# Kernel optimization log

Measured on AMD Instinct MI355X. Metric: run time of the kernel, lower is better.

The kernel has to match this reference:

```python
import jax, jax.numpy as jnp
import numpy as np

D = 1024      # d_model
H = 16        # nhead
DH = D // H   # d_head = 64
DC = D // 4   # d_compress = 256
HID = 2048    # dim_feedforward (SwiGLU hidden)
G = 2         # num_groups
EPG = 4       # experts_per_gp
E = G * EPG   # num_experts = 8
TOPK = 2
EPS = 1e-6
B, T = 2, 2048


def _rope_sincos(t, dh):
    inv_freq = 1.0 / (10000.0 ** (jnp.arange(0, dh, 2, dtype=jnp.float32) / dh))
    ang = jnp.arange(t, dtype=jnp.float32)[:, None] * inv_freq[None, :]  # [T, dh/2]
    return jnp.sin(ang), jnp.cos(ang)


def _apply_rope(x, sin, cos):
    # x: [B, H, T, DH]; sin/cos: [T, DH/2] broadcast over B,H
    x1 = x[..., ::2]
    x2 = x[..., 1::2]
    r = jnp.stack([x1 * cos - x2 * sin, x1 * sin + x2 * cos], axis=-1)
    return r.reshape(x.shape)


def _swiglu(x):
    a, b = jnp.split(x, 2, axis=-1)
    return jax.nn.silu(a) * b


def _rmsnorm(x, w):
    return x * jax.lax.rsqrt(jnp.mean(x * x, axis=-1, keepdims=True) + EPS) * w


def reference(src, Wq, Wk_c, Wv_c, Wk, Wv, Wo,
              W_shared_in, W_shared_out, W1_shared, W2_experts,
              Wg_gate, We_gate, group_bias, expert_bias, norm1_w, norm2_w):
    Bb, Tt, C = src.shape
    # ---- Latent attention (K/V compressed to d_c then re-expanded) ----
    q = (src @ Wq).reshape(Bb, Tt, H, DH).transpose(0, 2, 1, 3)
    k = ((src @ Wk_c) @ Wk).reshape(Bb, Tt, H, DH).transpose(0, 2, 1, 3)
    v = ((src @ Wv_c) @ Wv).reshape(Bb, Tt, H, DH).transpose(0, 2, 1, 3)
    sin, cos = _rope_sincos(Tt, DH)
    q = _apply_rope(q, sin, cos)
    k = _apply_rope(k, sin, cos)
    attn = jnp.einsum('bhqd,bhkd->bhqk', q, k) / np.sqrt(DH).astype(np.float32)
    attn = jax.nn.softmax(attn, axis=-1)
    sa = jnp.einsum('bhqk,bhkd->bhqd', attn, v)
    sa = sa.transpose(0, 2, 1, 3).reshape(Bb, Tt, C) @ Wo
    x = _rmsnorm(src + sa, norm1_w)

    # ---- Hierarchical MoE FFN ----
    S = Bb * Tt
    flat = x.reshape(S, C)
    shared = _swiglu(flat @ W_shared_in) @ W_shared_out          # [S, C]
    g_probs = jax.nn.softmax(flat @ Wg_gate + group_bias, -1)    # [S, G]
    g_idx = jnp.argmax(g_probs, axis=-1)                          # [S]
    e_logits = flat @ We_gate + expert_bias                       # [S, E]
    e_group = jnp.arange(E) // EPG
    in_group = e_group[None, :] == g_idx[:, None]                 # [S, E]
    e_probs = jax.nn.softmax(jnp.where(in_group, e_logits, -jnp.inf), -1)
    g_prob = jnp.take_along_axis(g_probs, g_idx[:, None], axis=1)  # [S, 1]
    p_expert = e_probs * g_prob
    topv, topi = jax.lax.top_k(p_expert, TOPK)                    # [S, K]
    # dense combine weights: zero for non-selected experts (same math as dispatch loop)
    w = jnp.zeros((S, E), flat.dtype).at[jnp.arange(S)[:, None], topi].set(topv)
    h = _swiglu(flat @ W1_shared)                                 # [S, HID] (w1 shared by all experts)
    routed = jnp.zeros_like(shared)
    for e in range(E):  # fixed small expert count
        routed = routed + (h @ W2_experts[e]) * w[:, e:e + 1]
    out = x + (shared + routed).reshape(Bb, Tt, C)
    return _rmsnorm(out, norm2_w)


def setup_inputs() -> dict:
    key = jax.random.key(0)
    ks = jax.random.split(key, 14)
    s = 0.02
    return {
        'src': jax.random.normal(ks[0], (B, T, D), jnp.float32),
        'Wq': jax.random.normal(ks[1], (D, D), jnp.float32) * s,
        'Wk_c': jax.random.normal(ks[2], (D, DC), jnp.float32) * s,
        'Wv_c': jax.random.normal(ks[3], (D, DC), jnp.float32) * s,
        'Wk': jax.random.normal(ks[4], (DC, D), jnp.float32) * s,
        'Wv': jax.random.normal(ks[5], (DC, D), jnp.float32) * s,
        'Wo': jax.random.normal(ks[6], (D, D), jnp.float32) * s,
        'W_shared_in': jax.random.normal(ks[7], (D, 2 * HID), jnp.float32) * s,
        'W_shared_out': jax.random.normal(ks[8], (HID, D), jnp.float32) * s,
        'W1_shared': jax.random.normal(ks[9], (D, 2 * HID), jnp.float32) * s,
        'W2_experts': jax.random.normal(ks[10], (E, HID, D), jnp.float32) * s,
        'Wg_gate': jax.random.normal(ks[11], (D, G), jnp.float32) * s,
        'We_gate': jax.random.normal(ks[12], (D, E), jnp.float32) * s,
        'group_bias': jnp.zeros((G,), jnp.float32),
        'expert_bias': jnp.zeros((E,), jnp.float32),
        'norm1_w': jnp.ones((D,), jnp.float32),
        'norm2_w': jnp.ones((D,), jnp.float32),
    }
```

## Files before the change

### kernel.cpp

```cpp
#include <hip/hip_runtime.h>
#include <math.h>

#define D_    1024
#define H_    16
#define DH_   64
#define DC_   256
#define HID_  2048
#define E_    8
#define B_    2
#define T_    2048
#define S_    4096
#define EPS_  1e-6f
#define QKVW_ 3072

typedef unsigned short u16;
typedef short bf16x8 __attribute__((ext_vector_type(8)));
typedef float f32x4 __attribute__((ext_vector_type(4)));

__device__ __forceinline__ float b2f(u16 u) {
    return __uint_as_float(((unsigned int)u) << 16);
}
__device__ __forceinline__ u16 f2b(float f) {
    unsigned int u = __float_as_uint(f);
    u += 0x7FFF + ((u >> 16) & 1);
    return (u16)(u >> 16);
}
__device__ __forceinline__ void g2l16(const u16* g, u16* l) {
    __builtin_amdgcn_global_load_lds(
        (const __attribute__((address_space(1))) void*)g,
        (__attribute__((address_space(3))) void*)l, 16, 0, 0);
}

__global__ __launch_bounds__(256) void conv_t(const float* __restrict__ in,
                                              u16* __restrict__ out,
                                              int K, int N,
                                              long inZ, long outZ, int perm) {
    in  += (long)blockIdx.z * inZ;
    out += (long)blockIdx.z * outZ;
    __shared__ float t[32][33];
    const int n0 = blockIdx.x * 32, k0 = blockIdx.y * 32;
    int src_n0 = n0;
    if (perm) {
        int t64 = n0 >> 6;
        src_n0 = ((n0 & 63) == 0) ? t64 * 32 : (N / 2 + t64 * 32);
    }
    const int tx = threadIdx.x & 31, ty = threadIdx.x >> 5;
#pragma unroll
    for (int i = 0; i < 4; i++)
        t[ty + 8 * i][tx] = in[(long)(k0 + ty + 8 * i) * N + src_n0 + tx];
    __syncthreads();
#pragma unroll
    for (int i = 0; i < 4; i++)
        out[(long)(n0 + ty + 8 * i) * K + k0 + tx] = f2b(t[tx][ty + 8 * i]);
}

__global__ __launch_bounds__(256) void vt_conv(const u16* __restrict__ qkv,
                                               u16* __restrict__ vt) {
    __shared__ u16 t[32][34];
    const int bh = blockIdx.z;
    const int b = bh >> 4, h = bh & 15;
    const int t0 = blockIdx.x * 32, d0 = blockIdx.y * 32;
    const int tx = threadIdx.x & 31, ty = threadIdx.x >> 5;
#pragma unroll
    for (int i = 0; i < 4; i++)
        t[ty + 8 * i][tx] =
            qkv[((long)b * T_ + t0 + ty + 8 * i) * QKVW_ + 2048 + h * 64 + d0 + tx];
    __syncthreads();
#pragma unroll
    for (int i = 0; i < 4; i++)
        vt[((long)bh * 64 + d0 + ty + 8 * i) * T_ + t0 + tx] = t[tx][ty + 8 * i];
}

__global__ __launch_bounds__(256) void convert_bf16(const float* __restrict__ in,
                                                    u16* __restrict__ out, int n4) {
    int i = blockIdx.x * 256 + threadIdx.x;
    if (i >= n4) return;
    float4 f = ((const float4*)in)[i];
    ushort4 o;
    o.x = f2b(f.x); o.y = f2b(f.y); o.z = f2b(f.z); o.w = f2b(f.w);
    ((ushort4*)out)[i] = o;
}

template<int OUTMODE>
__global__ __launch_bounds__(256) void gemm_bf16(const u16* __restrict__ A,
                                                 const u16* __restrict__ Bt,
                                                 void* __restrict__ Cp,
                                                 int N, int K, int ldo,
                                                 void* __restrict__ Cp2) {
    __shared__ u16 As[128 * 32];
    __shared__ u16 Bs[128 * 32];
    const int tid  = threadIdx.x;
    const int lane = tid & 63;
    const int wv   = tid >> 6;
    const int wm   = wv >> 1, wn = wv & 1;
    const long row0 = (long)blockIdx.y * 128;
    const long col0 = (long)blockIdx.x * 128;
    const int Klocal = K / gridDim.z;
    const long koff  = (long)blockIdx.z * Klocal;

    f32x4 acc[4][4];
#pragma unroll
    for (int i = 0; i < 4; i++)
#pragma unroll
        for (int j = 0; j < 4; j++) acc[i][j] = (f32x4){0.f, 0.f, 0.f, 0.f};

    const int sr = tid >> 2;
    const int sc = (tid & 3) << 3;
    const u16* Ag  = A  + (row0 + sr) * (long)K + koff + sc;
    const u16* Ag2 = Ag + 64 * (long)K;
    const u16* Bg  = Bt + (col0 + sr) * (long)K + koff + sc;
    const u16* Bg2 = Bg + 64 * (long)K;
    u16* lA  = As + tid * 8;
    u16* lA2 = As + 2048 + tid * 8;
    u16* lB  = Bs + tid * 8;
    u16* lB2 = Bs + 2048 + tid * 8;

    const int fl = lane & 15;
    const int fk = (lane >> 4) << 3;
    const u16* ArA = As + (wm * 64 + fl) * 32 + fk;
    const u16* BrB = Bs + (wn * 64 + fl) * 32 + fk;

    for (int k0 = 0; k0 < Klocal; k0 += 32) {
        __syncthreads();
        g2l16(Ag + k0, lA);
        g2l16(Ag2 + k0, lA2);
        g2l16(Bg + k0, lB);
        g2l16(Bg2 + k0, lB2);
        __syncthreads();
        bf16x8 af[4], bfr[4];
#pragma unroll
        for (int mi = 0; mi < 4; mi++) af[mi]  = *(const bf16x8*)(ArA + mi * 512);
#pragma unroll
        for (int ni = 0; ni < 4; ni++) bfr[ni] = *(const bf16x8*)(BrB + ni * 512);
#pragma unroll
        for (int mi = 0; mi < 4; mi++)
#pragma unroll
            for (int ni = 0; ni < 4; ni++)
                acc[mi][ni] = __builtin_amdgcn_mfma_f32_16x16x32_bf16(
                    af[mi], bfr[ni], acc[mi][ni], 0, 0, 0);
    }

    const int cr = (lane >> 4) << 2;
    const int cc = lane & 15;
#pragma unroll
    for (int mi = 0; mi < 4; mi++) {
#pragma unroll
        for (int r = 0; r < 4; r++) {
            long grow = row0 + wm * 64 + mi * 16 + cr + r;
#pragma unroll
            for (int ni = 0; ni < 4; ni++) {
                long gcol = col0 + wn * 64 + ni * 16 + cc;
                float v = acc[mi][ni][r];
                if (OUTMODE == 1)      ((u16*)Cp)[grow * ldo + gcol] = f2b(v);
                else if (OUTMODE == 2) ((u16*)Cp)[gcol * ldo + grow] = f2b(v);
                else {
                    float* basep = (float*)(blockIdx.z ? Cp2 : Cp);
                    basep[grow * ldo + gcol] = v;
                }
            }
        }
    }
}

template<int OUTMODE>
__global__ __launch_bounds__(512) void gemm256(const u16* __restrict__ A,
                                               const u16* __restrict__ Bt,
                                               void* __restrict__ Cp,
                                               int K, int ldo) {
    __shared__ u16 As[2][256 * 64];
    __shared__ u16 Bs[2][256 * 64];
    const int tid  = threadIdx.x;
    const int lane = tid & 63;
    const int w    = tid >> 6;
    const int wr   = w >> 2, wc = w & 3;
    const long row0 = (long)blockIdx.y * 256;
    const long col0 = (long)blockIdx.x * 256;

    f32x4 acc[8][4];
#pragma unroll
    for (int i = 0; i < 8; i++)
#pragma unroll
        for (int j = 0; j < 4; j++) acc[i][j] = (f32x4){0.f, 0.f, 0.f, 0.f};

    const int srow = tid >> 3;
    const int sgS  = ((tid & 7) ^ (srow & 7)) << 3;
    const u16* Ag = A  + (row0 + srow) * (long)K + sgS;
    const u16* Bg = Bt + (col0 + srow) * (long)K + sgS;

    const int fl = lane & 15;
    const int fq = lane >> 4;
    const int aoff = (wr * 128 + fl) * 64;
    const int boff = (wc * 64 + fl) * 64;

#define STAGE256(j, buf) do {                                             \
        const long ko_ = (long)(j) * 64;                                  \
        u16* la_ = As[buf] + tid * 8;                                     \
        u16* lb_ = Bs[buf] + tid * 8;                                     \
        _Pragma("unroll")                                                 \
        for (int rr_ = 0; rr_ < 4; rr_++)                                 \
            g2l16(Ag + (long)rr_ * 64 * K + ko_, la_ + rr_ * 4096);       \
        _Pragma("unroll")                                                 \
        for (int rr_ = 0; rr_ < 4; rr_++)                                 \
            g2l16(Bg + (long)rr_ * 64 * K + ko_, lb_ + rr_ * 4096);       \
    } while (0)

    STAGE256(0, 0);
    __syncthreads();
    const int NT = K >> 6;
    for (int j = 0; j < NT; j++) {
        const int buf = j & 1;
        if (j + 1 < NT) STAGE256(j + 1, buf ^ 1);
        const u16* ab = As[buf];
        const u16* bb = Bs[buf];
#pragma unroll
        for (int ks = 0; ks < 2; ks++) {
            const int sw = ((ks * 4 + fq) ^ (fl & 7)) << 3;
            bf16x8 af[8], bfr[4];
#pragma unroll
            for (int mi = 0; mi < 8; mi++)
                af[mi] = *(const bf16x8*)(ab + aoff + mi * 1024 + sw);
#pragma unroll
            for (int ni = 0; ni < 4; ni++)
                bfr[ni] = *(const bf16x8*)(bb + boff + ni * 1024 + sw);
#pragma unroll
            for (int mi = 0; mi < 8; mi++)
#pragma unroll
                for (int ni = 0; ni < 4; ni++)
                    acc[mi][ni] = __builtin_amdgcn_mfma_f32_16x16x32_bf16(
                        af[mi], bfr[ni], acc[mi][ni], 0, 0, 0);
        }
        __syncthreads();
    }

    const int cr = fq << 2;
    const int cc = fl;
#pragma unroll
    for (int mi = 0; mi < 8; mi++) {
#pragma unroll
        for (int r = 0; r < 4; r++) {
            long grow = row0 + wr * 128 + mi * 16 + cr + r;
            if (OUTMODE == 3) {
                u16* outb = (u16*)Cp + (long)(blockIdx.x >> 4) * S_ * HID_;
                u16* hrow = outb + grow * ldo + (blockIdx.x & 15) * 128 + wc * 32;
#pragma unroll
                for (int ni = 0; ni < 2; ni++) {
                    float a = acc[mi][ni][r], b = acc[mi][ni + 2][r];
                    float sig = 1.f / (1.f + __expf(-a));
                    hrow[ni * 16 + cc] = f2b(a * sig * b);
                }
            } else {
#pragma unroll
                for (int ni = 0; ni < 4; ni++) {
                    long gcol = col0 + wc * 64 + ni * 16 + cc;
                    ((u16*)Cp)[grow * ldo + gcol] = f2b(acc[mi][ni][r]);
                }
            }
        }
    }
#undef STAGE256
}

__global__ __launch_bounds__(256) void routed_gemm(const u16* __restrict__ Hh,
                                                   const u16* __restrict__ W2T,
                                                   const int* __restrict__ list,
                                                   const float* __restrict__ wlist,
                                                   const int* __restrict__ bases,
                                                   const int* __restrict__ counts,
                                                   float* __restrict__ Cout) {
    const int e    = blockIdx.y >> 5;
    const int tile = blockIdx.y & 31;
    const int cnt  = counts[e];
    if (tile * 128 >= cnt) return;
    const int base = bases[e];

    __shared__ u16 As[128 * 32];
    __shared__ u16 Bs[128 * 32];
    __shared__ int   toks[128];
    __shared__ float wrow[128];

    const int tid = threadIdx.x;
    if (tid < 128) {
        int ridx = tile * 128 + tid;
        if (ridx < cnt) { toks[tid] = list[base + ridx]; wrow[tid] = wlist[base + ridx]; }
        else            { toks[tid] = -1;                wrow[tid] = 0.f; }
    }
    __syncthreads();

    const int lane = tid & 63;
    const int wv   = tid >> 6;
    const int wm   = wv >> 1, wn = wv & 1;
    const long col0 = (long)blockIdx.x * 128;

    f32x4 acc[4][4];
#pragma unroll
    for (int i = 0; i < 4; i++)
#pragma unroll
        for (int j = 0; j < 4; j++) acc[i][j] = (f32x4){0.f, 0.f, 0.f, 0.f};

    const int sr = tid >> 2;
    const int sc = (tid & 3) << 3;
    const int t1 = toks[sr], t2 = toks[sr + 64];
    const u16* Ag  = Hh + (long)(t1 < 0 ? 0 : t1) * HID_ + sc;
    const u16* Ag2 = Hh + (long)(t2 < 0 ? 0 : t2) * HID_ + sc;
    const u16* Bg  = W2T + (long)e * D_ * HID_ + (col0 + sr) * (long)HID_ + sc;
    const u16* Bg2 = Bg + 64 * (long)HID_;
    u16* lA  = As + tid * 8;
    u16* lA2 = As + 2048 + tid * 8;
    u16* lB  = Bs + tid * 8;
    u16* lB2 = Bs + 2048 + tid * 8;

    const int fl = lane & 15;
    const int fk = (lane >> 4) << 3;
    const u16* ArA = As + (wm * 64 + fl) * 32 + fk;
    const u16* BrB = Bs + (wn * 64 + fl) * 32 + fk;

    for (int k0 = 0; k0 < HID_; k0 += 32) {
        __syncthreads();
        g2l16(Ag + k0, lA);
        g2l16(Ag2 + k0, lA2);
        g2l16(Bg + k0, lB);
        g2l16(Bg2 + k0, lB2);
        __syncthreads();
        bf16x8 af[4], bfr[4];
#pragma unroll
        for (int mi = 0; mi < 4; mi++) af[mi]  = *(const bf16x8*)(ArA + mi * 512);
#pragma unroll
        for (int ni = 0; ni < 4; ni++) bfr[ni] = *(const bf16x8*)(BrB + ni * 512);
#pragma unroll
        for (int mi = 0; mi < 4; mi++)
#pragma unroll
            for (int ni = 0; ni < 4; ni++)
                acc[mi][ni] = __builtin_amdgcn_mfma_f32_16x16x32_bf16(
                    af[mi], bfr[ni], acc[mi][ni], 0, 0, 0);
    }

    const int cr = (lane >> 4) << 2;
    const int cc = lane & 15;
#pragma unroll
    for (int mi = 0; mi < 4; mi++) {
#pragma unroll
        for (int r = 0; r < 4; r++) {
            int rr = wm * 64 + mi * 16 + cr + r;
            int tk = toks[rr];
            if (tk < 0) continue;
            float wvw = wrow[rr];
            float* crow = Cout + (long)tk * D_ + col0 + wn * 64;
#pragma unroll
            for (int ni = 0; ni < 4; ni++)
                atomicAdd(crow + ni * 16 + cc, acc[mi][ni][r] * wvw);
        }
    }
}

__global__ __launch_bounds__(256) void rope_table(float2* __restrict__ tab) {
    int idx = blockIdx.x * 256 + threadIdx.x;
    int t = idx >> 5, i = idx & 31;
    float ang = (float)t * powf(10000.f, -(float)i / 32.f);
    float sn, cs;
    sincosf(ang, &sn, &cs);
    tab[idx] = make_float2(sn, cs);
}

__global__ __launch_bounds__(256) void rope_apply(u16* __restrict__ qkv,
                                                  const float2* __restrict__ tab) {
    long p = (long)blockIdx.x * 256 + threadIdx.x;
    int s  = (int)(p >> 8);
    int c8 = (int)(p & 255) << 3;
    int t  = s & (T_ - 1);
    const float2* tp = tab + t * 32 + ((c8 & 63) >> 1);
    u16* px = qkv + (long)s * QKVW_ + c8;
    bf16x8 v = *(const bf16x8*)px;
    bf16x8 o;
#pragma unroll
    for (int j = 0; j < 4; j++) {
        float x1 = b2f((u16)v[2 * j]), x2 = b2f((u16)v[2 * j + 1]);
        float2 sc = tp[j];
        o[2 * j]     = (short)f2b(x1 * sc.y - x2 * sc.x);
        o[2 * j + 1] = (short)f2b(x1 * sc.x + x2 * sc.y);
    }
    *(bf16x8*)px = o;
}

__global__ __launch_bounds__(512) void attn_kernel(const u16* __restrict__ qkv,
                                                   const u16* __restrict__ vtg,
                                                   u16* __restrict__ sab) {
    __shared__ u16 Ks[128 * 64];
    __shared__ u16 Vs[64 * 128];
    __shared__ u16 Ps[8][16 * 128];
    const int tid  = threadIdx.x;
    const int lane = tid & 63;
    const int w    = tid >> 6;
    const int flat = blockIdx.x + (blockIdx.y << 4);
    const int virt = ((flat & 7) << 6) | (flat >> 3);
    const int qt = virt & 15;
    const int bh = virt >> 4;
    const int b  = bh >> 4, h = bh & 15;
    const long tok0 = (long)b * T_ + qt * 128;
    const int fl = lane & 15;
    const int fq = lane >> 4;

    bf16x8 qf0, qf1;
    {
        const u16* qp = qkv + (tok0 + w * 16 + fl) * QKVW_ + h * 64 + fq * 8;
        qf0 = *(const bf16x8*)qp;
        qf1 = *(const bf16x8*)(qp + 32);
    }

    const u16* kb0 = qkv + ((long)b * T_) * QKVW_ + 1024 + h * 64;
    const u16* vb0 = vtg + ((long)bh * 64) * T_;

    const int kr0 = tid >> 3,         kgg = tid & 7;
    const int kr1 = (tid + 512) >> 3;
    const int vr0 = tid >> 4,         vgg = tid & 15;
    const int vr1 = (tid + 512) >> 4;
    const u16* kp0 = kb0 + (long)kr0 * QKVW_ + ((kgg ^ (kr0 & 7)) << 3);
    const u16* kp1 = kb0 + (long)kr1 * QKVW_ + ((kgg ^ (kr1 & 7)) << 3);
    const u16* vp0 = vb0 + (long)vr0 * T_ + ((vgg ^ (vr0 & 15)) << 3);
    const u16* vp1 = vb0 + (long)vr1 * T_ + ((vgg ^ (vr1 & 15)) << 3);
    u16* kl0 = Ks + tid * 8;
    u16* kl1 = Ks + (tid + 512) * 8;
    u16* vl0 = Vs + tid * 8;
    u16* vl1 = Vs + (tid + 512) * 8;

    bf16x8 kreg0, kreg1, vreg0, vreg1;
    auto stage_load = [&](int kt) {
        const long ko = (long)kt * 128 * QKVW_;
        const int  vo = kt * 128;
        kreg0 = *(const bf16x8*)(kp0 + ko);
        kreg1 = *(const bf16x8*)(kp1 + ko);
        vreg0 = *(const bf16x8*)(vp0 + vo);
        vreg1 = *(const bf16x8*)(vp1 + vo);
    };
    auto stage_write = [&]() {
        *(bf16x8*)kl0 = kreg0;
        *(bf16x8*)kl1 = kreg1;
        *(bf16x8*)vl0 = vreg0;
        *(bf16x8*)vl1 = vreg1;
    };

    float m_[4], l_[4];
    f32x4 oacc[4];
#pragma unroll
    for (int i = 0; i < 4; i++) {
        m_[i] = -1e30f; l_[i] = 0.f;
        oacc[i] = (f32x4){0.f, 0.f, 0.f, 0.f};
    }

    stage_load(0);
    stage_write();
    __syncthreads();

    for (int kt = 0; kt < T_ / 128; kt++) {
        const bool pf = (kt + 1 < T_ / 128);
        if (pf) stage_load(kt + 1);

        f32x4 sacc[8];
#pragma unroll
        for (int ni = 0; ni < 8; ni++) sacc[ni] = (f32x4){0.f, 0.f, 0.f, 0.f};
        __builtin_amdgcn_s_setprio(1);
#pragma unroll
        for (int ks = 0; ks < 2; ks++) {
            bf16x8 qq = ks ? qf1 : qf0;
#pragma unroll
            for (int ni = 0; ni < 8; ni++) {
                bf16x8 kf = *(const bf16x8*)(Ks + (ni * 16 + fl) * 64 +
                                             (((ks * 4 + fq) ^ (fl & 7)) << 3));
                sacc[ni] = __builtin_amdgcn_mfma_f32_16x16x32_bf16(qq, kf, sacc[ni], 0, 0, 0);
            }
        }
        __builtin_amdgcn_s_setprio(0);

        float rmax[4];
#pragma unroll
        for (int r = 0; r < 4; r++) {
            float mm = sacc[0][r];
#pragma unroll
            for (int ni = 1; ni < 8; ni++) mm = fmaxf(mm, sacc[ni][r]);
            rmax[r] = mm * 0.125f;
        }
#pragma unroll
        for (int off = 1; off < 16; off <<= 1)
#pragma unroll
            for (int r = 0; r < 4; r++) rmax[r] = fmaxf(rmax[r], __shfl_xor(rmax[r], off));

        bool grow = false;
        float nm[4];
#pragma unroll
        for (int r = 0; r < 4; r++) {
            nm[r] = fmaxf(m_[r], rmax[r]);
            grow = grow || (rmax[r] > m_[r] + 8.f);
        }
        if (__any(grow)) {
#pragma unroll
            for (int r = 0; r < 4; r++) {
                float a = __expf(m_[r] - nm[r]);
                m_[r] = nm[r];
                l_[r] *= a;
#pragma unroll
                for (int ni = 0; ni < 4; ni++) oacc[ni][r] *= a;
            }
        }

        float psum[4];
#pragma unroll
        for (int r = 0; r < 4; r++) psum[r] = 0.f;
        u16* pst = Ps[w];
#pragma unroll
        for (int ni = 0; ni < 8; ni++) {
            int colg = ni * 2 + (fl >> 3);
            int cl   = fl & 7;
#pragma unroll
            for (int r = 0; r < 4; r++) {
                int row = fq * 4 + r;
                float p = __expf(sacc[ni][r] * 0.125f - m_[r]);
                psum[r] += p;
                pst[row * 128 + ((colg ^ (row & 15)) << 3) + cl] = f2b(p);
            }
        }
#pragma unroll
        for (int off = 1; off < 16; off <<= 1)
#pragma unroll
            for (int r = 0; r < 4; r++) psum[r] += __shfl_xor(psum[r], off);
#pragma unroll
        for (int r = 0; r < 4; r++) l_[r] += psum[r];

        __builtin_amdgcn_s_setprio(1);
#pragma unroll
        for (int ks = 0; ks < 4; ks++) {
            bf16x8 pfr = *(const bf16x8*)(pst + fl * 128 +
                                          (((ks * 4 + fq) ^ fl) << 3));
#pragma unroll
            for (int ni = 0; ni < 4; ni++) {
                bf16x8 vf = *(const bf16x8*)(Vs + (ni * 16 + fl) * 128 +
                                             (((ks * 4 + fq) ^ fl) << 3));
                oacc[ni] = __builtin_amdgcn_mfma_f32_16x16x32_bf16(pfr, vf, oacc[ni], 0, 0, 0);
            }
        }
        __builtin_amdgcn_s_setprio(0);

        __syncthreads();
        if (pf) {
            stage_write();
            __syncthreads();
        }
    }

#pragma unroll
    for (int r = 0; r < 4; r++) {
        float inv = 1.f / l_[r];
        u16* op = sab + (tok0 + w * 16 + fq * 4 + r) * D_ + h * 64 + fl;
#pragma unroll
        for (int ni = 0; ni < 4; ni++) op[ni * 16] = f2b(oacc[ni][r] * inv);
    }
}

template<int BF>
__global__ __launch_bounds__(256) void rmsnorm_res(const float* __restrict__ a,
                                                   const float* __restrict__ b,
                                                   const float* __restrict__ b2,
                                                   const float* __restrict__ w,
                                                   float* __restrict__ outf,
                                                   u16* __restrict__ outb) {
    const int s = blockIdx.x;
    const float* ar = a + (long)s * D_;
    const float* br = b + (long)s * D_;
    const float* cr2 = b2 + (long)s * D_;
    float y[4];
    float ss = 0.f;
#pragma unroll
    for (int kx = 0; kx < 4; kx++) {
        int j = threadIdx.x + kx * 256;
        y[kx] = ar[j] + br[j] + cr2[j];
        ss += y[kx] * y[kx];
    }
    __shared__ float red[4];
#pragma unroll
    for (int off = 32; off > 0; off >>= 1) ss += __shfl_down(ss, off);
    int lane = threadIdx.x & 63, wv = threadIdx.x >> 6;
    if (lane == 0) red[wv] = ss;
    __syncthreads();
    float tot = red[0] + red[1] + red[2] + red[3];
    float scl = rsqrtf(tot / (float)D_ + EPS_);
    float* orow = outf + (long)s * D_;
#pragma unroll
    for (int kx = 0; kx < 4; kx++) {
        int j = threadIdx.x + kx * 256;
        float v = y[kx] * scl * w[j];
        orow[j] = v;
        if (BF) outb[(long)s * D_ + j] = f2b(v);
    }
}

__global__ __launch_bounds__(256) void gate_kernel(const float* __restrict__ x,
                                                   const float* __restrict__ Wg,
                                                   const float* __restrict__ We,
                                                   const float* __restrict__ gb,
                                                   const float* __restrict__ eb,
                                                   int* __restrict__ tok_e,
                                                   float* __restrict__ tok_w) {
    const int wave = threadIdx.x >> 6;
    const int lane = threadIdx.x & 63;
    const int s = blockIdx.x * 4 + wave;
    const float* xr = x + (long)s * D_;
    float g0 = 0.f, g1 = 0.f;
    float ee[8];
#pragma unroll
    for (int e = 0; e < 8; e++) ee[e] = 0.f;
    for (int j = lane; j < D_; j += 64) {
        float xv = xr[j];
        g0 += xv * Wg[j * 2 + 0];
        g1 += xv * Wg[j * 2 + 1];
#pragma unroll
        for (int e = 0; e < 8; e++) ee[e] += xv * We[j * 8 + e];
    }
#pragma unroll
    for (int off = 32; off > 0; off >>= 1) {
        g0 += __shfl_down(g0, off);
        g1 += __shfl_down(g1, off);
#pragma unroll
        for (int e = 0; e < 8; e++) ee[e] += __shfl_down(ee[e], off);
    }
    if (lane == 0) {
        g0 += gb[0];
        g1 += gb[1];
        int gidx = (g1 > g0) ? 1 : 0;
        float gm = fmaxf(g0, g1);
        float p0 = expf(g0 - gm), p1 = expf(g1 - gm);
        float gprob = (gidx ? p1 : p0) / (p0 + p1);
        int base = gidx * 4;
        float pe[4];
        float em = -1e30f;
#pragma unroll
        for (int i = 0; i < 4; i++) {
            pe[i] = ee[base + i] + eb[base + i];
            em = fmaxf(em, pe[i]);
        }
        float sum = 0.f;
#pragma unroll
        for (int i = 0; i < 4; i++) { pe[i] = expf(pe[i] - em); sum += pe[i]; }
        float inv = gprob / sum;
#pragma unroll
        for (int i = 0; i < 4; i++) pe[i] *= inv;
        int i1 = 0;
        for (int i = 1; i < 4; i++) if (pe[i] > pe[i1]) i1 = i;
        int i2 = -1;
        for (int i = 0; i < 4; i++) {
            if (i == i1) continue;
            if (i2 < 0 || pe[i] > pe[i2]) i2 = i;
        }
        tok_e[s * 2 + 0] = base + i1;
        tok_e[s * 2 + 1] = base + i2;
        tok_w[s * 2 + 0] = pe[i1];
        tok_w[s * 2 + 1] = pe[i2];
    }
}

__global__ __launch_bounds__(256) void route_build(const int* __restrict__ tok_e,
                                                   const float* __restrict__ tok_w,
                                                   int* __restrict__ counts_g,
                                                   int* __restrict__ bases_g,
                                                   int* __restrict__ list,
                                                   float* __restrict__ wlist) {
    __shared__ int cnt[E_], bas[E_], cur[E_];
    const int tid = threadIdx.x;
    if (tid < E_) cnt[tid] = 0;
    __syncthreads();
    for (int i = tid; i < 2 * S_; i += 256) atomicAdd(&cnt[tok_e[i]], 1);
    __syncthreads();
    if (tid == 0) {
        int acc = 0;
        for (int e = 0; e < E_; e++) { bas[e] = acc; cur[e] = acc; acc += cnt[e]; }
    }
    __syncthreads();
    if (tid < E_) { counts_g[tid] = cnt[tid]; bases_g[tid] = bas[tid]; }
    for (int i = tid; i < 2 * S_; i += 256) {
        int e = tok_e[i];
        int p = atomicAdd(&cur[e], 1);
        list[p] = i >> 1;
        wlist[p] = tok_w[i];
    }
}

extern "C" void kernel_launch(void* const* d_in, const int* in_sizes, int n_in,
                              void* d_out, int out_size, void* d_ws, size_t ws_size,
                              hipStream_t stream) {
    const float* src  = (const float*)d_in[0];
    const float* Wq   = (const float*)d_in[1];
    const float* Wk_c = (const float*)d_in[2];
    const float* Wv_c = (const float*)d_in[3];
    const float* Wk   = (const float*)d_in[4];
    const float* Wv   = (const float*)d_in[5];
    const float* Wo   = (const float*)d_in[6];
    const float* Wsin = (const float*)d_in[7];
    const float* Wsout= (const float*)d_in[8];
    const float* W1   = (const float*)d_in[9];
    const float* W2   = (const float*)d_in[10];
    const float* Wg   = (const float*)d_in[11];
    const float* We   = (const float*)d_in[12];
    const float* gb   = (const float*)d_in[13];
    const float* eb   = (const float*)d_in[14];
    const float* n1w  = (const float*)d_in[15];
    const float* n2w  = (const float*)d_in[16];
    float* out = (float*)d_out;

    const size_t MB = 1u << 20;
    char* w8 = (char*)d_ws;
    u16*  qkv   = (u16*)(w8);
    u16*  vtg   = (u16*)(w8 + 24 * MB);
    float* oproj0 = (float*)(w8);
    float* oproj1 = (float*)(w8 + 16 * MB);
    u16*  w2t   = (u16*)(w8);
    u16*  WkcB  = (u16*)(w8 + 24 * MB);
    u16*  WvcB  = (u16*)(w8 + 24 * MB + 512 * 1024);
    u16*  WkTs  = (u16*)(w8 + 25 * MB);
    u16*  WvTs  = (u16*)(w8 + 25 * MB + 512 * 1024);
    u16*  sab   = (u16*)(w8 + 32 * MB);
    float* tokw = (float*)(w8 + 32 * MB);
    float* wlist = tokw + 2 * S_;
    int* toke   = (int*)(wlist + 2 * S_);
    int* list   = toke + 2 * S_;
    int* counts = list + 2 * S_;
    int* bases  = counts + E_;
    float* x1   = (float*)(w8 + 40 * MB);
    float* ffn0 = (float*)(w8 + 56 * MB);
    u16*  x1b   = (u16*)(w8 + 72 * MB);
    u16*  hbuf  = (u16*)(w8 + 80 * MB);
    u16*  srcb  = (u16*)(w8 + 96 * MB);
    float2* rtab= (float2*)(w8 + 104 * MB);
    u16*  hbuf2 = (u16*)(w8 + 96 * MB);
    u16*  WqkvT = (u16*)(w8 + 112 * MB);
    u16*  WsoutT= (u16*)(w8 + 112 * MB);
    u16*  WoT   = (u16*)(w8 + 118 * MB);
    u16*  WsinT = (u16*)(w8 + 120 * MB);
    u16*  W1T   = (u16*)(w8 + 128 * MB);
    float* ffn1 = (float*)(w8 + 120 * MB);

    dim3 blk(256);

    conv_t<<<dim3(32, 32), blk, 0, stream>>>(Wq, WqkvT, 1024, 1024, 0, 0, 0);
    convert_bf16<<<dim3(D_ * DC_ / 4 / 256), blk, 0, stream>>>(Wk_c, WkcB, D_ * DC_ / 4);
    convert_bf16<<<dim3(D_ * DC_ / 4 / 256), blk, 0, stream>>>(Wv_c, WvcB, D_ * DC_ / 4);
    conv_t<<<dim3(32, 8), blk, 0, stream>>>(Wk, WkTs, 256, 1024, 0, 0, 0);
    conv_t<<<dim3(32, 8), blk, 0, stream>>>(Wv, WvTs, 256, 1024, 0, 0, 0);
    gemm_bf16<2><<<dim3(8, 8), blk, 0, stream>>>(WkcB, WkTs, WqkvT + 1024 * 1024, 1024, 256, 1024, nullptr);
    gemm_bf16<2><<<dim3(8, 8), blk, 0, stream>>>(WvcB, WvTs, WqkvT + 2048 * 1024, 1024, 256, 1024, nullptr);

    convert_bf16<<<dim3(S_ * D_ / 4 / 256), blk, 0, stream>>>(src, srcb, S_ * D_ / 4);

    gemm256<1><<<dim3(QKVW_ / 256, S_ / 256), dim3(512), 0, stream>>>(srcb, WqkvT, qkv, 1024, QKVW_);

    conv_t<<<dim3(32, 32), blk, 0, stream>>>(Wo, WoT, 1024, 1024, 0, 0, 0);
    conv_t<<<dim3(128, 32), blk, 0, stream>>>(Wsin, WsinT, 1024, 4096, 0, 0, 1);
    conv_t<<<dim3(32, 64), blk, 0, stream>>>(Wsout, WsoutT, 2048, 1024, 0, 0, 0);
    conv_t<<<dim3(128, 32), blk, 0, stream>>>(W1, W1T, 1024, 4096, 0, 0, 1);

    rope_table<<<dim3(T_ * 32 / 256), blk, 0, stream>>>(rtab);
    rope_apply<<<dim3(S_ * 2048 / 8 / 256), blk, 0, stream>>>(qkv, rtab);

    vt_conv<<<dim3(T_ / 32, 2, B_ * H_), blk, 0, stream>>>(qkv, vtg);
    attn_kernel<<<dim3(T_ / 128, B_ * H_), dim3(512), 0, stream>>>(qkv, vtg, sab);

    gemm_bf16<5><<<dim3(8, 32, 2), blk, 0, stream>>>(sab, WoT, oproj0, 1024, 1024, 1024, oproj1);
    rmsnorm_res<1><<<dim3(S_), blk, 0, stream>>>(src, oproj0, oproj1, n1w, x1, x1b);

    gemm256<3><<<dim3(8192 / 256, S_ / 256), dim3(512), 0, stream>>>(x1b, WsinT, hbuf, 1024, 2048);

    gemm_bf16<5><<<dim3(8, 32, 2), blk, 0, stream>>>(hbuf, WsoutT, ffn0, 1024, 2048, 1024, ffn1);

    gate_kernel<<<dim3(S_ / 4), blk, 0, stream>>>(x1, Wg, We, gb, eb, toke, tokw);
    route_build<<<dim3(1), blk, 0, stream>>>(toke, tokw, counts, bases, list, wlist);

    conv_t<<<dim3(32, 64, 8), blk, 0, stream>>>(W2, w2t, 2048, 1024,
                                                (long)HID_ * D_, (long)D_ * HID_, 0);
    routed_gemm<<<dim3(8, E_ * 32), blk, 0, stream>>>(hbuf2, w2t, list, wlist,
                                                      bases, counts, ffn0);

    rmsnorm_res<0><<<dim3(S_), blk, 0, stream>>>(x1, ffn0, ffn1, n2w, out, (u16*)nullptr);
}
```

Baseline: 631.7 us.

## Add double-buffered swizzled 128x128 GEMM and pipeline routed expert GEMM

Adds a new 128x128 split-K GEMM kernel with a BK=64 double-buffered LDS pipeline and XOR-swizzled shared-memory layout. It replaces the older gemm_bf16<5> kernel for the output projection and the shared FFN down-projection. The routed expert GEMM gets the same restructuring, going from single-buffered BK=32 tiles with two barriers per step to prefetching the next tile while computing the current one. The aim is to hide global-load latency and cut LDS bank conflicts, at the cost of four times the shared memory per block (64 KB), which may lower occupancy.

```diff
diff --git a/kernel.cpp b/kernel.cpp
--- a/kernel.cpp
+++ b/kernel.cpp
@@ -260,6 +260,95 @@
 #undef STAGE256
 }
 
+__global__ __launch_bounds__(256) void gemm128p(const u16* __restrict__ A,
+                                                const u16* __restrict__ Bt,
+                                                float* __restrict__ Cp,
+                                                int K, int ldo,
+                                                float* __restrict__ Cp2) {
+    __shared__ u16 As[2][128 * 64];
+    __shared__ u16 Bs[2][128 * 64];
+    const int tid  = threadIdx.x;
+    const int lane = tid & 63;
+    const int wv   = tid >> 6;
+    const int wm   = wv >> 1, wn = wv & 1;
+    const long row0 = (long)blockIdx.y * 128;
+    const long col0 = (long)blockIdx.x * 128;
+    const int Klocal = K / gridDim.z;
+    const long koff  = (long)blockIdx.z * Klocal;
+
+    f32x4 acc[4][4];
+#pragma unroll
+    for (int i = 0; i < 4; i++)
+#pragma unroll
+        for (int j = 0; j < 4; j++) acc[i][j] = (f32x4){0.f, 0.f, 0.f, 0.f};
+
+    const int srow = tid >> 3;
+    const int sgS  = ((tid & 7) ^ (srow & 7)) << 3;
+    const u16* Ag = A  + (row0 + srow) * (long)K + koff + sgS;
+    const u16* Bg = Bt + (col0 + srow) * (long)K + koff + sgS;
+
+    const int fl = lane & 15;
+    const int fq = lane >> 4;
+    const int aoff = (wm * 64 + fl) * 64;
+    const int boff = (wn * 64 + fl) * 64;
+
+#define STAGE128(j, buf) do {                                             \
+        const long ko_ = (long)(j) * 64;                                  \
+        u16* la_ = As[buf] + tid * 8;                                     \
+        u16* lb_ = Bs[buf] + tid * 8;                                     \
+        _Pragma("unroll")                                                 \
+        for (int rr_ = 0; rr_ < 4; rr_++)                                 \
+            g2l16(Ag + (long)rr_ * 32 * K + ko_, la_ + rr_ * 2048);       \
+        _Pragma("unroll")                                                 \
+        for (int rr_ = 0; rr_ < 4; rr_++)                                 \
+            g2l16(Bg + (long)rr_ * 32 * K + ko_, lb_ + rr_ * 2048);       \
+    } while (0)
+
+    STAGE128(0, 0);
+    __syncthreads();
+    const int NT = Klocal >> 6;
+    for (int j = 0; j < NT; j++) {
+        const int buf = j & 1;
+        if (j + 1 < NT) STAGE128(j + 1, buf ^ 1);
+        const u16* ab = As[buf];
+        const u16* bb = Bs[buf];
+#pragma unroll
+        for (int ks = 0; ks < 2; ks++) {
+            const int sw = ((ks * 4 + fq) ^ (fl & 7)) << 3;
+            bf16x8 af[4], bfr[4];
+#pragma unroll
+            for (int mi = 0; mi < 4; mi++)
+                af[mi] = *(const bf16x8*)(ab + aoff + mi * 1024 + sw);
+#pragma unroll
+            for (int ni = 0; ni < 4; ni++)
+                bfr[ni] = *(const bf16x8*)(bb + boff + ni * 1024 + sw);
+#pragma unroll
+            for (int mi = 0; mi < 4; mi++)
+#pragma unroll
+                for (int ni = 0; ni < 4; ni++)
+                    acc[mi][ni] = __builtin_amdgcn_mfma_f32_16x16x32_bf16(
+                        af[mi], bfr[ni], acc[mi][ni], 0, 0, 0);
+        }
+        __syncthreads();
+    }
+
+    float* basep = blockIdx.z ? Cp2 : Cp;
+    const int cr = fq << 2;
+#pragma unroll
+    for (int mi = 0; mi < 4; mi++) {
+#pragma unroll
+        for (int r = 0; r < 4; r++) {
+            long grow = row0 + wm * 64 + mi * 16 + cr + r;
+#pragma unroll
+            for (int ni = 0; ni < 4; ni++) {
+                long gcol = col0 + wn * 64 + ni * 16 + fl;
+                basep[grow * ldo + gcol] = acc[mi][ni][r];
+            }
+        }
+    }
+#undef STAGE128
+}
+
 __global__ __launch_bounds__(256) void routed_gemm(const u16* __restrict__ Hh,
                                                    const u16* __restrict__ W2T,
                                                    const int* __restrict__ list,
@@ -273,8 +362,8 @@
     if (tile * 128 >= cnt) return;
     const int base = bases[e];
 
-    __shared__ u16 As[128 * 32];
-    __shared__ u16 Bs[128 * 32];
+    __shared__ u16 As[2][128 * 64];
+    __shared__ u16 Bs[2][128 * 64];
     __shared__ int   toks[128];
     __shared__ float wrow[128];
 
@@ -297,45 +386,63 @@
 #pragma unroll
         for (int j = 0; j < 4; j++) acc[i][j] = (f32x4){0.f, 0.f, 0.f, 0.f};
 
-    const int sr = tid >> 2;
-    const int sc = (tid & 3) << 3;
-    const int t1 = toks[sr], t2 = toks[sr + 64];
-    const u16* Ag  = Hh + (long)(t1 < 0 ? 0 : t1) * HID_ + sc;
-    const u16* Ag2 = Hh + (long)(t2 < 0 ? 0 : t2) * HID_ + sc;
-    const u16* Bg  = W2T + (long)e * D_ * HID_ + (col0 + sr) * (long)HID_ + sc;
-    const u16* Bg2 = Bg + 64 * (long)HID_;
-    u16* lA  = As + tid * 8;
-    u16* lA2 = As + 2048 + tid * 8;
-    u16* lB  = Bs + tid * 8;
-    u16* lB2 = Bs + 2048 + tid * 8;
+    const int srow = tid >> 3;
+    const int sgS  = ((tid & 7) ^ (srow & 7)) << 3;
+    const u16* Apt[4];
+#pragma unroll
+    for (int rr = 0; rr < 4; rr++) {
+        int t = toks[srow + 32 * rr];
+        Apt[rr] = Hh + (long)(t < 0 ? 0 : t) * HID_ + sgS;
+    }
+    const u16* Bg = W2T + (long)e * D_ * HID_ + (col0 + srow) * (long)HID_ + sgS;
 
     const int fl = lane & 15;
-    const int fk = (lane >> 4) << 3;
-    const u16* ArA = As + (wm * 64 + fl) * 32 + fk;
-    const u16* BrB = Bs + (wn * 64 + fl) * 32 + fk;
-
-    for (int k0 = 0; k0 < HID_; k0 += 32) {
+    const int fq = lane >> 4;
+    const int aoff = (wm * 64 + fl) * 64;
+    const int boff = (wn * 64 + fl) * 64;
+
+#define STAGER(j, buf) do {                                               \
+        const long ko_ = (long)(j) * 64;                                  \
+        u16* la_ = As[buf] + tid * 8;                                     \
+        u16* lb_ = Bs[buf] + tid * 8;                                     \
+        _Pragma("unroll")                                                 \
+        for (int rr_ = 0; rr_ < 4; rr_++)                                 \
+            g2l16(Apt[rr_] + ko_, la_ + rr_ * 2048);                      \
+        _Pragma("unroll")                                                 \
+        for (int rr_ = 0; rr_ < 4; rr_++)                                 \
+            g2l16(Bg + (long)rr_ * 32 * HID_ + ko_, lb_ + rr_ * 2048);    \
+    } while (0)
+
+    STAGER(0, 0);
+    __syncthreads();
+    const int NT = HID_ >> 6;
+    for (int j = 0; j < NT; j++) {
+        const int buf = j & 1;
+        if (j + 1 < NT) STAGER(j + 1, buf ^ 1);
+        const u16* ab = As[buf];
+        const u16* bb = Bs[buf];
+#pragma unroll
+        for (int ks = 0; ks < 2; ks++) {
+            const int sw = ((ks * 4 + fq) ^ (fl & 7)) << 3;
+            bf16x8 af[4], bfr[4];
+#pragma unroll
+            for (int mi = 0; mi < 4; mi++)
+                af[mi] = *(const bf16x8*)(ab + aoff + mi * 1024 + sw);
+#pragma unroll
+            for (int ni = 0; ni < 4; ni++)
+                bfr[ni] = *(const bf16x8*)(bb + boff + ni * 1024 + sw);
+#pragma unroll
+            for (int mi = 0; mi < 4; mi++)
+#pragma unroll
+                for (int ni = 0; ni < 4; ni++)
+                    acc[mi][ni] = __builtin_amdgcn_mfma_f32_16x16x32_bf16(
+                        af[mi], bfr[ni], acc[mi][ni], 0, 0, 0);
+        }
         __syncthreads();
-        g2l16(Ag + k0, lA);
-        g2l16(Ag2 + k0, lA2);
-        g2l16(Bg + k0, lB);
-        g2l16(Bg2 + k0, lB2);
-        __syncthreads();
-        bf16x8 af[4], bfr[4];
-#pragma unroll
-        for (int mi = 0; mi < 4; mi++) af[mi]  = *(const bf16x8*)(ArA + mi * 512);
-#pragma unroll
-        for (int ni = 0; ni < 4; ni++) bfr[ni] = *(const bf16x8*)(BrB + ni * 512);
-#pragma unroll
-        for (int mi = 0; mi < 4; mi++)
-#pragma unroll
-            for (int ni = 0; ni < 4; ni++)
-                acc[mi][ni] = __builtin_amdgcn_mfma_f32_16x16x32_bf16(
-                    af[mi], bfr[ni], acc[mi][ni], 0, 0, 0);
-    }
-
-    const int cr = (lane >> 4) << 2;
-    const int cc = lane & 15;
+    }
+
+    const int cr = fq << 2;
+    const int cc = fl;
 #pragma unroll
     for (int mi = 0; mi < 4; mi++) {
 #pragma unroll
@@ -350,6 +457,7 @@
                 atomicAdd(crow + ni * 16 + cc, acc[mi][ni][r] * wvw);
         }
     }
+#undef STAGER
 }
 
 __global__ __launch_bounds__(256) void rope_table(float2* __restrict__ tab) {
@@ -760,12 +868,12 @@
     vt_conv<<<dim3(T_ / 32, 2, B_ * H_), blk, 0, stream>>>(qkv, vtg);
     attn_kernel<<<dim3(T_ / 128, B_ * H_), dim3(512), 0, stream>>>(qkv, vtg, sab);
 
-    gemm_bf16<5><<<dim3(8, 32, 2), blk, 0, stream>>>(sab, WoT, oproj0, 1024, 1024, 1024, oproj1);
+    gemm128p<<<dim3(8, 32, 2), blk, 0, stream>>>(sab, WoT, oproj0, 1024, 1024, oproj1);
     rmsnorm_res<1><<<dim3(S_), blk, 0, stream>>>(src, oproj0, oproj1, n1w, x1, x1b);
 
     gemm256<3><<<dim3(8192 / 256, S_ / 256), dim3(512), 0, stream>>>(x1b, WsinT, hbuf, 1024, 2048);
 
-    gemm_bf16<5><<<dim3(8, 32, 2), blk, 0, stream>>>(hbuf, WsoutT, ffn0, 1024, 2048, 1024, ffn1);
+    gemm128p<<<dim3(8, 32, 2), blk, 0, stream>>>(hbuf, WsoutT, ffn0, 2048, 1024, ffn1);
 
     gate_kernel<<<dim3(S_ / 4), blk, 0, stream>>>(x1, Wg, We, gb, eb, toke, tokw);
     route_build<<<dim3(1), blk, 0, stream>>>(toke, tokw, counts, bases, list, wlist);
```

Measured after the change: 657.9 us. 1.04x slower.
